# Kernel optimization log

Measured on AMD Instinct MI355X. Metric: run time of the kernel, lower is better.

The kernel has to match this reference:

```python
import jax, jax.numpy as jnp
import numpy as np

COEFS = [1.5, 1.2, 1.0, 0.9, 0.82, 0.69, 0.65, 0.56]  # self.coefs reversed
COMMITMENT_COST = 0.4


def number_to_pair(n):
    if n == 1:
        return (0, 1)
    m = (n - 1) // 2
    e = 1 if (n % 2 == 0) else 0
    return (2 * m + 3 + e - 1, 2 * m + 4 + e - 1)


def build_codebooks(weight, num_levels):
    # Level-l codebook has 2^l vectors, built as sums of pairs of rows of `weight`.
    d = weight.shape[1]
    cbs = []
    prev = None
    for stage in range(1, num_levels + 1):
        i0, i1 = number_to_pair(stage)
        vecs = weight[i0:i1 + 1]            # [2, d]
        if stage == 1:
            cb = vecs
        else:
            cb = (prev[:, None, :] + vecs[None, :, :]).reshape(-1, d)
        cbs.append(cb)
        prev = cb
    return cbs


def quantize(cb, flat):
    dists = (jnp.sum(flat ** 2, axis=1, keepdims=True)
             + jnp.sum(cb ** 2, axis=1)
             - 2.0 * flat @ cb.T)           # [N, K]
    idx = jnp.argmin(dists, axis=1)          # [N]
    return jnp.take(cb, idx, axis=0)         # == one-hot @ cb


def setup_inputs() -> dict:
    key = jax.random.key(0)
    k1, k2 = jax.random.split(key)
    B, d, H, W = 16, 128, 64, 64
    p = 256
    inputs = jax.random.normal(k1, (B, d, H, W), dtype=jnp.float32)
    weight = jax.random.normal(k2, (p, d), dtype=jnp.float32)  # nn.Embedding default N(0,1)
    return {"inputs": inputs, "weight": weight, "num_vectors": 256}


def reference(inputs, weight, num_vectors):
    num_levels = int(np.log2(num_vectors))   # 8
    x = jnp.transpose(inputs, (0, 2, 3, 1))  # [B, H, W, d]
    d = x.shape[-1]
    flat = x.reshape(-1, d)                  # [N, d]
    cbs = build_codebooks(weight, num_levels)

    quant_vecs = []
    losses = []
    for level in range(num_levels):
        q = quantize(cbs[level], flat).reshape(x.shape)
        e_latent = jnp.mean((jax.lax.stop_gradient(q) - x) ** 2)
        q_latent = jnp.mean((jax.lax.stop_gradient(x) - q) ** 2)
        losses.append(COEFS[level] * q_latent + COMMITMENT_COST * e_latent)
        st = x + jax.lax.stop_gradient(q - x)             # straight-through
        quant_vecs.append(jnp.transpose(st, (0, 3, 1, 2)))  # back to [B, d, H, W]

    return jnp.stack(quant_vecs), jnp.stack(losses)
```

## Files before the change

kernel.cpp:

```cpp
#include <hip/hip_runtime.h>

typedef unsigned long long u64;

#define OFF_A      0
#define OFF_DT     512
#define OFF_V0T    1536
#define OFF_BASET  2560
#define OFF_IDX_BYTES 16384
#define OFF_PART_F    135168

__device__ __forceinline__ float warp_sum(float v) {
  #pragma unroll
  for (int off = 32; off > 0; off >>= 1) v += __shfl_down(v, off);
  return v;
}

__global__ __launch_bounds__(64) void build_tables(const float* __restrict__ w,
                                                   float* __restrict__ wsf) {
  const int r0[8] = {0, 3, 4, 5, 6, 7, 8, 9};
  int e = blockIdx.x;
  int t = threadIdx.x;
  if (e < 510) {
    int ep2 = e + 2;
    int L = 31 - __clz(ep2);
    int i = ep2 - (1 << L);
    float acc = 0.f;
    #pragma unroll
    for (int half = 0; half < 2; ++half) {
      int cc = t + half * 64;
      float v = 0.f;
      for (int s = 0; s < L; ++s) {
        int b = (i >> (L - 1 - s)) & 1;
        v += w[(r0[s] + b) * 128 + cc];
      }
      acc += v * v;
    }
    acc = warp_sum(acc);
    if (t == 0) wsf[OFF_A + e] = -0.5f * acc;
  } else {
    #pragma unroll
    for (int half = 0; half < 2; ++half) {
      int cc = t + half * 64;
      float basesum = 0.f;
      #pragma unroll
      for (int s = 0; s < 8; ++s) {
        float w0 = w[r0[s] * 128 + cc];
        float w1 = w[(r0[s] + 1) * 128 + cc];
        wsf[OFF_V0T + cc * 8 + s] = w0;
        wsf[OFF_DT + cc * 8 + s] = w1 - w0;
        basesum += w0;
        wsf[OFF_BASET + s * 128 + cc] = basesum;
      }
    }
  }
}

template <int L, int I, int N>
struct SU {
  static __device__ __forceinline__ void run(const float* __restrict__ Al,
                                             const float* T, const float* S,
                                             float& bs, int& bi) {
    float dot;
    if constexpr (L <= 4) {
      dot = T[I << (4 - L)];
    } else {
      dot = T[I >> (L - 4)] + S[(I & ((1 << (L - 4)) - 1)) << (8 - L)];
    }
    float sc = dot + Al[I];
    if (sc > bs) { bs = sc; bi = I; }
    SU<L, I + 1, N>::run(Al, T, S, bs, bi);
  }
};
template <int L, int N>
struct SU<L, N, N> {
  static __device__ __forceinline__ void run(const float*, const float*, const float*,
                                             float&, int&) {}
};

template <int L>
__device__ __forceinline__ void search_level(const float* __restrict__ A,
                                             const float* T, const float* S,
                                             float& bestsc, int& bestidx) {
  const float* Al = A + ((1 << L) - 2);
  float bs = -3.4e38f;
  int bi = 0;
  SU<L, 0, (1 << L)>::run(Al, T, S, bs, bi);
  bestsc = bs;
  bestidx = bi;
}

__global__ __launch_bounds__(256) void search_kernel(const float* __restrict__ in,
                                                     const float* __restrict__ tbl,
                                                     float* __restrict__ partial,
                                                     u64* __restrict__ idxp) {
  __shared__ float red[4][8];
  int pos = blockIdx.x * 256 + threadIdx.x;
  int b = pos >> 12;
  int hw = pos & 4095;
  const float* xp = in + ((size_t)b << 19) + hw;
  const float4* dT4 = (const float4*)(tbl + OFF_DT);
  const float4* v04 = (const float4*)(tbl + OFF_V0T);

  float qq[8], uu[8];
  #pragma unroll
  for (int k = 0; k < 8; ++k) { qq[k] = 0.f; uu[k] = 0.f; }
  float xx = 0.f;
  #pragma unroll 4
  for (int c = 0; c < 128; ++c) {
    float x = xp[(size_t)c << 12];
    float4 d0 = dT4[2 * c];
    float4 d1 = dT4[2 * c + 1];
    float4 u0 = v04[2 * c];
    float4 u1 = v04[2 * c + 1];
    xx = fmaf(x, x, xx);
    qq[0] = fmaf(x, d0.x, qq[0]); qq[1] = fmaf(x, d0.y, qq[1]);
    qq[2] = fmaf(x, d0.z, qq[2]); qq[3] = fmaf(x, d0.w, qq[3]);
    qq[4] = fmaf(x, d1.x, qq[4]); qq[5] = fmaf(x, d1.y, qq[5]);
    qq[6] = fmaf(x, d1.z, qq[6]); qq[7] = fmaf(x, d1.w, qq[7]);
    uu[0] = fmaf(x, u0.x, uu[0]); uu[1] = fmaf(x, u0.y, uu[1]);
    uu[2] = fmaf(x, u0.z, uu[2]); uu[3] = fmaf(x, u0.w, uu[3]);
    uu[4] = fmaf(x, u1.x, uu[4]); uu[5] = fmaf(x, u1.y, uu[5]);
    uu[6] = fmaf(x, u1.z, uu[6]); uu[7] = fmaf(x, u1.w, uu[7]);
  }

  float T[16], S[16];
  #pragma unroll
  for (int h = 0; h < 16; ++h) {
    float tv = 0.f, sv = 0.f;
    if (h & 8) { tv += qq[0]; sv += qq[4]; }
    if (h & 4) { tv += qq[1]; sv += qq[5]; }
    if (h & 2) { tv += qq[2]; sv += qq[6]; }
    if (h & 1) { tv += qq[3]; sv += qq[7]; }
    T[h] = tv; S[h] = sv;
  }

  const float* A = tbl + OFF_A;
  float bsc[8];
  int bix[8];
  search_level<1>(A, T, S, bsc[0], bix[0]);
  search_level<2>(A, T, S, bsc[1], bix[1]);
  search_level<3>(A, T, S, bsc[2], bix[2]);
  search_level<4>(A, T, S, bsc[3], bix[3]);
  search_level<5>(A, T, S, bsc[4], bix[4]);
  search_level<6>(A, T, S, bsc[5], bix[5]);
  search_level<7>(A, T, S, bsc[6], bix[6]);
  search_level<8>(A, T, S, bsc[7], bix[7]);

  u64 pk = (u64)bix[0] | ((u64)bix[1] << 1) | ((u64)bix[2] << 3) | ((u64)bix[3] << 6) |
           ((u64)bix[4] << 10) | ((u64)bix[5] << 15) | ((u64)bix[6] << 21) |
           ((u64)bix[7] << 28);
  idxp[pos] = pk;

  int wv = threadIdx.x >> 6;
  float P0 = 0.f;
  #pragma unroll
  for (int l = 0; l < 8; ++l) {
    P0 += uu[l];
    float sse = xx - 2.f * (P0 + bsc[l]);
    sse = warp_sum(sse);
    if ((threadIdx.x & 63) == 0) red[wv][l] = sse;
  }
  __syncthreads();
  if (threadIdx.x < 8) {
    int l = threadIdx.x;
    partial[l * 256 + blockIdx.x] = red[0][l] + red[1][l] + red[2][l] + red[3][l];
  }
}

template <int LV>
__device__ __forceinline__ void write_level(const u64* __restrict__ idxp,
                                            const float* __restrict__ tbl,
                                            float* __restrict__ op, int pos) {
  const int SH[9] = {0, 0, 1, 3, 6, 10, 15, 21, 28};
  u64 pk = idxp[pos];
  int idx = (int)((pk >> SH[LV]) & ((1u << LV) - 1));
  float bf[LV];
  #pragma unroll
  for (int s = 0; s < LV; ++s) bf[s] = (float)((idx >> (LV - 1 - s)) & 1);
  const float* bt = tbl + OFF_BASET + (LV - 1) * 128;
  const float4* dT4 = (const float4*)(tbl + OFF_DT);
  #pragma unroll 4
  for (int c = 0; c < 128; ++c) {
    float qv = bt[c];
    float dv[8];
    float4 d0 = dT4[2 * c];
    dv[0] = d0.x; dv[1] = d0.y; dv[2] = d0.z; dv[3] = d0.w;
    if constexpr (LV > 4) {
      float4 d1 = dT4[2 * c + 1];
      dv[4] = d1.x; dv[5] = d1.y; dv[6] = d1.z; dv[7] = d1.w;
    }
    #pragma unroll
    for (int s = 0; s < LV; ++s) qv = fmaf(bf[s], dv[s], qv);
    op[(size_t)c << 12] = qv;
  }
}

__global__ __launch_bounds__(256) void write_kernel(const float* __restrict__ tbl,
                                                    const u64* __restrict__ idxp,
                                                    float* __restrict__ out) {
  int blk = blockIdx.x;
  int hb = blk & 15;
  int bb = (blk >> 4) & 15;
  int L = blk >> 8;
  int hw = hb * 256 + threadIdx.x;
  int pos = (bb << 12) + hw;
  float* op = out + (((size_t)(L * 16 + bb)) << 19) + hw;
  switch (L) {
    case 0: write_level<1>(idxp, tbl, op, pos); break;
    case 1: write_level<2>(idxp, tbl, op, pos); break;
    case 2: write_level<3>(idxp, tbl, op, pos); break;
    case 3: write_level<4>(idxp, tbl, op, pos); break;
    case 4: write_level<5>(idxp, tbl, op, pos); break;
    case 5: write_level<6>(idxp, tbl, op, pos); break;
    case 6: write_level<7>(idxp, tbl, op, pos); break;
    case 7: write_level<8>(idxp, tbl, op, pos); break;
  }
  if (blk == 0 && threadIdx.x < 64) {
    const float CO[8] = {1.5f, 1.2f, 1.0f, 0.9f, 0.82f, 0.69f, 0.65f, 0.56f};
    const float* partial = tbl + OFF_PART_F;
    int t = threadIdx.x;
    int l = t >> 3;
    int j = t & 7;
    float s = 0.f;
    #pragma unroll 4
    for (int k = 0; k < 32; ++k) s += partial[l * 256 + j + k * 8];
    s += __shfl_down(s, 4);
    s += __shfl_down(s, 2);
    s += __shfl_down(s, 1);
    if (j == 0)
      out[67108864ull + l] = (CO[l] + 0.4f) * s * (1.0f / 8388608.0f);
  }
}

extern "C" void kernel_launch(void* const* d_in, const int* in_sizes, int n_in,
                              void* d_out, int out_size, void* d_ws, size_t ws_size,
                              hipStream_t stream) {
  const float* in = (const float*)d_in[0];
  const float* w  = (const float*)d_in[1];
  float* wsf = (float*)d_ws;
  u64* idxp = (u64*)((char*)d_ws + OFF_IDX_BYTES);
  float* partial = wsf + OFF_PART_F;
  float* out = (float*)d_out;

  build_tables<<<511, 64, 0, stream>>>(w, wsf);
  search_kernel<<<256, 256, 0, stream>>>(in, wsf, partial, idxp);
  write_kernel<<<2048, 256, 0, stream>>>(wsf, idxp, out);
}
```

Before: 328.8 us.

## Split channel reduction and level search across waves; vectorize quantized output writes

The search kernel now uses four waves per block, each covering 64 positions. Each wave accumulates a quarter of the channels, the partial sums are reduced through shared memory, and the level searches are divided among the waves. This raises the search grid from 256 to 1024 blocks for more parallelism and memory-level concurrency. The tables are staged in LDS. The write kernel now has each thread produce four adjacent positions with float4 stores, using LDS-cached tables, which cuts the block count to 512. The costs are extra shared-memory traffic, extra barriers, and unbalanced search work across waves.

```diff
diff --git a/kernel.cpp b/kernel.cpp
--- a/kernel.cpp
+++ b/kernel.cpp
@@ -57,9 +57,8 @@
 
 template <int L, int I, int N>
 struct SU {
-  static __device__ __forceinline__ void run(const float* __restrict__ Al,
-                                             const float* T, const float* S,
-                                             float& bs, int& bi) {
+  static __device__ __forceinline__ void run(const float* Al, const float* T,
+                                             const float* S, float& bs, int& bi) {
     float dot;
     if constexpr (L <= 4) {
       dot = T[I << (4 - L)];
@@ -78,10 +77,9 @@
 };
 
 template <int L>
-__device__ __forceinline__ void search_level(const float* __restrict__ A,
-                                             const float* T, const float* S,
-                                             float& bestsc, int& bestidx) {
-  const float* Al = A + ((1 << L) - 2);
+__device__ __forceinline__ void search_level(const float* Al_base, const float* T,
+                                             const float* S, float& bestsc, int& bestidx) {
+  const float* Al = Al_base + ((1 << L) - 2);
   float bs = -3.4e38f;
   int bi = 0;
   SU<L, 0, (1 << L)>::run(Al, T, S, bs, bi);
@@ -93,34 +91,58 @@
                                                      const float* __restrict__ tbl,
                                                      float* __restrict__ partial,
                                                      u64* __restrict__ idxp) {
-  __shared__ float red[4][8];
-  int pos = blockIdx.x * 256 + threadIdx.x;
-  int b = pos >> 12;
-  int hw = pos & 4095;
-  const float* xp = in + ((size_t)b << 19) + hw;
-  const float4* dT4 = (const float4*)(tbl + OFF_DT);
-  const float4* v04 = (const float4*)(tbl + OFF_V0T);
+  __shared__ float dTl[1024];
+  __shared__ float v0l[1024];
+  __shared__ float Al[512];
+  __shared__ float part[256][17];
+  __shared__ float lsc[4][64];
+  __shared__ int   lix[4][64];
+
+  int tid = threadIdx.x;
+  for (int i = tid; i < 1024; i += 256) { dTl[i] = tbl[OFF_DT + i]; v0l[i] = tbl[OFF_V0T + i]; }
+  if (tid < 255) { Al[tid] = tbl[OFF_A + tid]; Al[tid + 255] = tbl[OFF_A + tid + 255]; }
+  __syncthreads();
+
+  int q = tid >> 6;
+  int posl = tid & 63;
+  int gpos = blockIdx.x * 64 + posl;
+  int b = gpos >> 12;
+  int hw = gpos & 4095;
+  const float* xp = in + ((size_t)b << 19) + ((size_t)(q * 32) << 12) + hw;
 
   float qq[8], uu[8];
   #pragma unroll
   for (int k = 0; k < 8; ++k) { qq[k] = 0.f; uu[k] = 0.f; }
   float xx = 0.f;
-  #pragma unroll 4
-  for (int c = 0; c < 128; ++c) {
-    float x = xp[(size_t)c << 12];
-    float4 d0 = dT4[2 * c];
-    float4 d1 = dT4[2 * c + 1];
-    float4 u0 = v04[2 * c];
-    float4 u1 = v04[2 * c + 1];
-    xx = fmaf(x, x, xx);
-    qq[0] = fmaf(x, d0.x, qq[0]); qq[1] = fmaf(x, d0.y, qq[1]);
-    qq[2] = fmaf(x, d0.z, qq[2]); qq[3] = fmaf(x, d0.w, qq[3]);
-    qq[4] = fmaf(x, d1.x, qq[4]); qq[5] = fmaf(x, d1.y, qq[5]);
-    qq[6] = fmaf(x, d1.z, qq[6]); qq[7] = fmaf(x, d1.w, qq[7]);
-    uu[0] = fmaf(x, u0.x, uu[0]); uu[1] = fmaf(x, u0.y, uu[1]);
-    uu[2] = fmaf(x, u0.z, uu[2]); uu[3] = fmaf(x, u0.w, uu[3]);
-    uu[4] = fmaf(x, u1.x, uu[4]); uu[5] = fmaf(x, u1.y, uu[5]);
-    uu[6] = fmaf(x, u1.z, uu[6]); uu[7] = fmaf(x, u1.w, uu[7]);
+  int cbase = q * 32;
+  float xv[16];
+  #pragma unroll
+  for (int g = 0; g < 2; ++g) {
+    #pragma unroll
+    for (int j = 0; j < 16; ++j) xv[j] = xp[(size_t)(g * 16 + j) << 12];
+    #pragma unroll
+    for (int j = 0; j < 16; ++j) {
+      float x = xv[j];
+      int c = cbase + g * 16 + j;
+      xx = fmaf(x, x, xx);
+      #pragma unroll
+      for (int k = 0; k < 8; ++k) {
+        qq[k] = fmaf(x, dTl[c * 8 + k], qq[k]);
+        uu[k] = fmaf(x, v0l[c * 8 + k], uu[k]);
+      }
+    }
+  }
+
+  #pragma unroll
+  for (int k = 0; k < 8; ++k) { part[tid][k] = qq[k]; part[tid][8 + k] = uu[k]; }
+  part[tid][16] = xx;
+  __syncthreads();
+  #pragma unroll
+  for (int p = 1; p < 4; ++p) {
+    int ptn = tid ^ (p << 6);
+    #pragma unroll
+    for (int k = 0; k < 8; ++k) { qq[k] += part[ptn][k]; uu[k] += part[ptn][8 + k]; }
+    xx += part[ptn][16];
   }
 
   float T[16], S[16];
@@ -134,87 +156,92 @@
     T[h] = tv; S[h] = sv;
   }
 
-  const float* A = tbl + OFF_A;
-  float bsc[8];
-  int bix[8];
-  search_level<1>(A, T, S, bsc[0], bix[0]);
-  search_level<2>(A, T, S, bsc[1], bix[1]);
-  search_level<3>(A, T, S, bsc[2], bix[2]);
-  search_level<4>(A, T, S, bsc[3], bix[3]);
-  search_level<5>(A, T, S, bsc[4], bix[4]);
-  search_level<6>(A, T, S, bsc[5], bix[5]);
-  search_level<7>(A, T, S, bsc[6], bix[6]);
-  search_level<8>(A, T, S, bsc[7], bix[7]);
-
-  u64 pk = (u64)bix[0] | ((u64)bix[1] << 1) | ((u64)bix[2] << 3) | ((u64)bix[3] << 6) |
-           ((u64)bix[4] << 10) | ((u64)bix[5] << 15) | ((u64)bix[6] << 21) |
-           ((u64)bix[7] << 28);
-  idxp[pos] = pk;
-
-  int wv = threadIdx.x >> 6;
-  float P0 = 0.f;
-  #pragma unroll
-  for (int l = 0; l < 8; ++l) {
-    P0 += uu[l];
-    float sse = xx - 2.f * (P0 + bsc[l]);
-    sse = warp_sum(sse);
-    if ((threadIdx.x & 63) == 0) red[wv][l] = sse;
-  }
-  __syncthreads();
-  if (threadIdx.x < 8) {
-    int l = threadIdx.x;
-    partial[l * 256 + blockIdx.x] = red[0][l] + red[1][l] + red[2][l] + red[3][l];
+  float bsc[4];
+  int bix[4];
+  if (q == 3) {
+    float bs; int bi;
+    search_level<8>(Al, T, S, bs, bi);
+    lsc[3][posl] = bs; lix[3][posl] = bi;
+  } else if (q == 2) {
+    float bs; int bi;
+    search_level<7>(Al, T, S, bs, bi);
+    lsc[2][posl] = bs; lix[2][posl] = bi;
+  } else if (q == 1) {
+    float bs; int bi;
+    search_level<5>(Al, T, S, bs, bi);
+    lsc[0][posl] = bs; lix[0][posl] = bi;
+    search_level<6>(Al, T, S, bs, bi);
+    lsc[1][posl] = bs; lix[1][posl] = bi;
+  } else {
+    search_level<1>(Al, T, S, bsc[0], bix[0]);
+    search_level<2>(Al, T, S, bsc[1], bix[1]);
+    search_level<3>(Al, T, S, bsc[2], bix[2]);
+    search_level<4>(Al, T, S, bsc[3], bix[3]);
+  }
+  __syncthreads();
+
+  if (q == 0) {
+    float s5 = lsc[0][posl], s6 = lsc[1][posl], s7 = lsc[2][posl], s8 = lsc[3][posl];
+    int i5 = lix[0][posl], i6 = lix[1][posl], i7 = lix[2][posl], i8 = lix[3][posl];
+    u64 pk = (u64)bix[0] | ((u64)bix[1] << 1) | ((u64)bix[2] << 3) | ((u64)bix[3] << 6) |
+             ((u64)i5 << 10) | ((u64)i6 << 15) | ((u64)i7 << 21) | ((u64)i8 << 28);
+    idxp[gpos] = pk;
+    float ball[8] = {bsc[0], bsc[1], bsc[2], bsc[3], s5, s6, s7, s8};
+    float P0 = 0.f;
+    #pragma unroll
+    for (int l = 0; l < 8; ++l) {
+      P0 += uu[l];
+      float sse = xx - 2.f * (P0 + ball[l]);
+      sse = warp_sum(sse);
+      if (tid == 0) partial[l * 1024 + blockIdx.x] = sse;
+    }
   }
 }
 
 template <int LV>
-__device__ __forceinline__ void write_level(const u64* __restrict__ idxp,
-                                            const float* __restrict__ tbl,
-                                            float* __restrict__ op, int pos) {
-  const int SH[9] = {0, 0, 1, 3, 6, 10, 15, 21, 28};
-  u64 pk = idxp[pos];
-  int idx = (int)((pk >> SH[LV]) & ((1u << LV) - 1));
-  float bf[LV];
-  #pragma unroll
-  for (int s = 0; s < LV; ++s) bf[s] = (float)((idx >> (LV - 1 - s)) & 1);
-  const float* bt = tbl + OFF_BASET + (LV - 1) * 128;
-  const float4* dT4 = (const float4*)(tbl + OFF_DT);
-  #pragma unroll 4
+__device__ __forceinline__ void write_level(const float* dTl, const float* btl,
+                                            const u64* __restrict__ idxp, int pos,
+                                            float4* __restrict__ op) {
+  constexpr int SHv = (LV == 1 ? 0 : LV == 2 ? 1 : LV == 3 ? 3 : LV == 4 ? 6 :
+                       LV == 5 ? 10 : LV == 6 ? 15 : LV == 7 ? 21 : 28);
+  float bf[4][LV];
+  #pragma unroll
+  for (int p = 0; p < 4; ++p) {
+    u64 pk = idxp[pos + p];
+    int idx = (int)((pk >> SHv) & ((1u << LV) - 1));
+    #pragma unroll
+    for (int s = 0; s < LV; ++s) bf[p][s] = (float)((idx >> (LV - 1 - s)) & 1);
+  }
+  #pragma unroll 2
   for (int c = 0; c < 128; ++c) {
-    float qv = bt[c];
-    float dv[8];
-    float4 d0 = dT4[2 * c];
-    dv[0] = d0.x; dv[1] = d0.y; dv[2] = d0.z; dv[3] = d0.w;
-    if constexpr (LV > 4) {
-      float4 d1 = dT4[2 * c + 1];
-      dv[4] = d1.x; dv[5] = d1.y; dv[6] = d1.z; dv[7] = d1.w;
-    }
-    #pragma unroll
-    for (int s = 0; s < LV; ++s) qv = fmaf(bf[s], dv[s], qv);
-    op[(size_t)c << 12] = qv;
+    float bt = btl[c];
+    float dv[LV];
+    #pragma unroll
+    for (int s = 0; s < LV; ++s) dv[s] = dTl[c * 8 + s];
+    float q0 = bt, q1 = bt, q2 = bt, q3 = bt;
+    #pragma unroll
+    for (int s = 0; s < LV; ++s) {
+      q0 = fmaf(bf[0][s], dv[s], q0);
+      q1 = fmaf(bf[1][s], dv[s], q1);
+      q2 = fmaf(bf[2][s], dv[s], q2);
+      q3 = fmaf(bf[3][s], dv[s], q3);
+    }
+    float4 r; r.x = q0; r.y = q1; r.z = q2; r.w = q3;
+    op[(size_t)c << 10] = r;
   }
 }
 
 __global__ __launch_bounds__(256) void write_kernel(const float* __restrict__ tbl,
                                                     const u64* __restrict__ idxp,
                                                     float* __restrict__ out) {
+  __shared__ float dTl[1024];
+  __shared__ float btl[128];
   int blk = blockIdx.x;
-  int hb = blk & 15;
-  int bb = (blk >> 4) & 15;
-  int L = blk >> 8;
-  int hw = hb * 256 + threadIdx.x;
-  int pos = (bb << 12) + hw;
-  float* op = out + (((size_t)(L * 16 + bb)) << 19) + hw;
-  switch (L) {
-    case 0: write_level<1>(idxp, tbl, op, pos); break;
-    case 1: write_level<2>(idxp, tbl, op, pos); break;
-    case 2: write_level<3>(idxp, tbl, op, pos); break;
-    case 3: write_level<4>(idxp, tbl, op, pos); break;
-    case 4: write_level<5>(idxp, tbl, op, pos); break;
-    case 5: write_level<6>(idxp, tbl, op, pos); break;
-    case 6: write_level<7>(idxp, tbl, op, pos); break;
-    case 7: write_level<8>(idxp, tbl, op, pos); break;
-  }
+  int L = blk >> 6;
+  for (int i = threadIdx.x; i < 1024; i += 256) dTl[i] = tbl[OFF_DT + i];
+  if (threadIdx.x < 128) btl[threadIdx.x] = tbl[OFF_BASET + L * 128 + threadIdx.x];
+  __syncthreads();
+
   if (blk == 0 && threadIdx.x < 64) {
     const float CO[8] = {1.5f, 1.2f, 1.0f, 0.9f, 0.82f, 0.69f, 0.65f, 0.56f};
     const float* partial = tbl + OFF_PART_F;
@@ -223,12 +250,28 @@
     int j = t & 7;
     float s = 0.f;
     #pragma unroll 4
-    for (int k = 0; k < 32; ++k) s += partial[l * 256 + j + k * 8];
+    for (int k = 0; k < 128; ++k) s += partial[l * 1024 + j + k * 8];
     s += __shfl_down(s, 4);
     s += __shfl_down(s, 2);
     s += __shfl_down(s, 1);
     if (j == 0)
       out[67108864ull + l] = (CO[l] + 0.4f) * s * (1.0f / 8388608.0f);
+  }
+
+  int g = (blk & 63) * 256 + threadIdx.x;
+  int pos = g << 2;
+  int bb = pos >> 12;
+  int hw = pos & 4095;
+  float4* op = (float4*)(out + (((size_t)(L * 16 + bb)) << 19) + hw);
+  switch (L) {
+    case 0: write_level<1>(dTl, btl, idxp, pos, op); break;
+    case 1: write_level<2>(dTl, btl, idxp, pos, op); break;
+    case 2: write_level<3>(dTl, btl, idxp, pos, op); break;
+    case 3: write_level<4>(dTl, btl, idxp, pos, op); break;
+    case 4: write_level<5>(dTl, btl, idxp, pos, op); break;
+    case 5: write_level<6>(dTl, btl, idxp, pos, op); break;
+    case 6: write_level<7>(dTl, btl, idxp, pos, op); break;
+    case 7: write_level<8>(dTl, btl, idxp, pos, op); break;
   }
 }
 
@@ -243,6 +286,6 @@
   float* out = (float*)d_out;
 
   build_tables<<<511, 64, 0, stream>>>(w, wsf);
-  search_kernel<<<256, 256, 0, stream>>>(in, wsf, partial, idxp);
-  write_kernel<<<2048, 256, 0, stream>>>(wsf, idxp, out);
-}
+  search_kernel<<<1024, 256, 0, stream>>>(in, wsf, partial, idxp);
+  write_kernel<<<512, 256, 0, stream>>>(wsf, idxp, out);
+}
```

Result: slower. 352.2 us (+7.1%).

## Fuse search and output-write kernels, stage tables in LDS, last-block loss reduction

Applied to the files above, without the earlier changes.

Merges the search and write kernels into one kernel where each thread computes its eight level indices and directly writes all eight straight-through outputs. This removes the packed-index round trip and a kernel launch. Lookup tables are staged in shared memory, and the final loss reduction runs in the last block to finish, found with an atomic counter. Each thread now does far more work, including 8x the stores, across only 512 blocks of 128 threads, which may reduce parallelism and memory-level concurrency for the write-heavy phase.

```diff
diff --git a/kernel.cpp b/kernel.cpp
--- a/kernel.cpp
+++ b/kernel.cpp
@@ -2,12 +2,12 @@
 
 typedef unsigned long long u64;
 
-#define OFF_A      0
-#define OFF_DT     512
-#define OFF_V0T    1536
-#define OFF_BASET  2560
-#define OFF_IDX_BYTES 16384
-#define OFF_PART_F    135168
+#define OFF_A    0
+#define OFF_DT   512
+#define OFF_V0T  1536
+#define OFF_BTT  2560
+#define OFF_PART 3584
+#define OFF_CNT  7680
 
 __device__ __forceinline__ float warp_sum(float v) {
   #pragma unroll
@@ -49,17 +49,17 @@
         wsf[OFF_V0T + cc * 8 + s] = w0;
         wsf[OFF_DT + cc * 8 + s] = w1 - w0;
         basesum += w0;
-        wsf[OFF_BASET + s * 128 + cc] = basesum;
+        wsf[OFF_BTT + cc * 8 + s] = basesum;
       }
     }
+    if (t == 0) ((int*)wsf)[OFF_CNT] = 0;
   }
 }
 
 template <int L, int I, int N>
 struct SU {
-  static __device__ __forceinline__ void run(const float* __restrict__ Al,
-                                             const float* T, const float* S,
-                                             float& bs, int& bi) {
+  static __device__ __forceinline__ void run(const float* Al, const float* T,
+                                             const float* S, float& bs, int& bi) {
     float dot;
     if constexpr (L <= 4) {
       dot = T[I << (4 - L)];
@@ -78,10 +78,9 @@
 };
 
 template <int L>
-__device__ __forceinline__ void search_level(const float* __restrict__ A,
-                                             const float* T, const float* S,
-                                             float& bestsc, int& bestidx) {
-  const float* Al = A + ((1 << L) - 2);
+__device__ __forceinline__ void search_level(const float* Al_base, const float* T,
+                                             const float* S, float& bestsc, int& bestidx) {
+  const float* Al = Al_base + ((1 << L) - 2);
   float bs = -3.4e38f;
   int bi = 0;
   SU<L, 0, (1 << L)>::run(Al, T, S, bs, bi);
@@ -89,17 +88,33 @@
   bestidx = bi;
 }
 
-__global__ __launch_bounds__(256) void search_kernel(const float* __restrict__ in,
-                                                     const float* __restrict__ tbl,
-                                                     float* __restrict__ partial,
-                                                     u64* __restrict__ idxp) {
-  __shared__ float red[4][8];
-  int pos = blockIdx.x * 256 + threadIdx.x;
-  int b = pos >> 12;
-  int hw = pos & 4095;
+__global__ __launch_bounds__(128) void fused_kernel(const float* __restrict__ in,
+                                                    const float* __restrict__ tbl,
+                                                    float* __restrict__ partial,
+                                                    int* __restrict__ counter,
+                                                    float* __restrict__ out) {
+  __shared__ __align__(16) float dTl[1024];
+  __shared__ __align__(16) float v0l[1024];
+  __shared__ __align__(16) float btl[1024];
+  __shared__ float Al[510];
+  __shared__ float red[2][8];
+  __shared__ int lastflag;
+
+  int tid = threadIdx.x;
+  for (int i = tid; i < 1024; i += 128) {
+    dTl[i] = tbl[OFF_DT + i];
+    v0l[i] = tbl[OFF_V0T + i];
+    btl[i] = tbl[OFF_BTT + i];
+  }
+  for (int i = tid; i < 510; i += 128) Al[i] = tbl[OFF_A + i];
+  __syncthreads();
+
+  int gpos = blockIdx.x * 128 + tid;
+  int b = gpos >> 12;
+  int hw = gpos & 4095;
   const float* xp = in + ((size_t)b << 19) + hw;
-  const float4* dT4 = (const float4*)(tbl + OFF_DT);
-  const float4* v04 = (const float4*)(tbl + OFF_V0T);
+  const float4* dT4 = (const float4*)dTl;
+  const float4* v04 = (const float4*)v0l;
 
   float qq[8], uu[8];
   #pragma unroll
@@ -108,10 +123,8 @@
   #pragma unroll 4
   for (int c = 0; c < 128; ++c) {
     float x = xp[(size_t)c << 12];
-    float4 d0 = dT4[2 * c];
-    float4 d1 = dT4[2 * c + 1];
-    float4 u0 = v04[2 * c];
-    float4 u1 = v04[2 * c + 1];
+    float4 d0 = dT4[2 * c], d1 = dT4[2 * c + 1];
+    float4 u0 = v04[2 * c], u1 = v04[2 * c + 1];
     xx = fmaf(x, x, xx);
     qq[0] = fmaf(x, d0.x, qq[0]); qq[1] = fmaf(x, d0.y, qq[1]);
     qq[2] = fmaf(x, d0.z, qq[2]); qq[3] = fmaf(x, d0.w, qq[3]);
@@ -134,101 +147,78 @@
     T[h] = tv; S[h] = sv;
   }
 
-  const float* A = tbl + OFF_A;
   float bsc[8];
   int bix[8];
-  search_level<1>(A, T, S, bsc[0], bix[0]);
-  search_level<2>(A, T, S, bsc[1], bix[1]);
-  search_level<3>(A, T, S, bsc[2], bix[2]);
-  search_level<4>(A, T, S, bsc[3], bix[3]);
-  search_level<5>(A, T, S, bsc[4], bix[4]);
-  search_level<6>(A, T, S, bsc[5], bix[5]);
-  search_level<7>(A, T, S, bsc[6], bix[6]);
-  search_level<8>(A, T, S, bsc[7], bix[7]);
-
-  u64 pk = (u64)bix[0] | ((u64)bix[1] << 1) | ((u64)bix[2] << 3) | ((u64)bix[3] << 6) |
-           ((u64)bix[4] << 10) | ((u64)bix[5] << 15) | ((u64)bix[6] << 21) |
-           ((u64)bix[7] << 28);
-  idxp[pos] = pk;
-
-  int wv = threadIdx.x >> 6;
+  search_level<1>(Al, T, S, bsc[0], bix[0]);
+  search_level<2>(Al, T, S, bsc[1], bix[1]);
+  search_level<3>(Al, T, S, bsc[2], bix[2]);
+  search_level<4>(Al, T, S, bsc[3], bix[3]);
+  search_level<5>(Al, T, S, bsc[4], bix[4]);
+  search_level<6>(Al, T, S, bsc[5], bix[5]);
+  search_level<7>(Al, T, S, bsc[6], bix[6]);
+  search_level<8>(Al, T, S, bsc[7], bix[7]);
+
+  int wv = tid >> 6;
   float P0 = 0.f;
   #pragma unroll
   for (int l = 0; l < 8; ++l) {
     P0 += uu[l];
     float sse = xx - 2.f * (P0 + bsc[l]);
     sse = warp_sum(sse);
-    if ((threadIdx.x & 63) == 0) red[wv][l] = sse;
-  }
-  __syncthreads();
-  if (threadIdx.x < 8) {
-    int l = threadIdx.x;
-    partial[l * 256 + blockIdx.x] = red[0][l] + red[1][l] + red[2][l] + red[3][l];
-  }
-}
-
-template <int LV>
-__device__ __forceinline__ void write_level(const u64* __restrict__ idxp,
-                                            const float* __restrict__ tbl,
-                                            float* __restrict__ op, int pos) {
-  const int SH[9] = {0, 0, 1, 3, 6, 10, 15, 21, 28};
-  u64 pk = idxp[pos];
-  int idx = (int)((pk >> SH[LV]) & ((1u << LV) - 1));
-  float bf[LV];
-  #pragma unroll
-  for (int s = 0; s < LV; ++s) bf[s] = (float)((idx >> (LV - 1 - s)) & 1);
-  const float* bt = tbl + OFF_BASET + (LV - 1) * 128;
-  const float4* dT4 = (const float4*)(tbl + OFF_DT);
-  #pragma unroll 4
+    if ((tid & 63) == 0) red[wv][l] = sse;
+  }
+  __syncthreads();
+  if (tid < 8) partial[tid * 512 + blockIdx.x] = red[0][tid] + red[1][tid];
+
+  const int TRI[8] = {0, 1, 3, 6, 10, 15, 21, 28};
+  float bf[36];
+  #pragma unroll
+  for (int l = 0; l < 8; ++l) {
+    #pragma unroll
+    for (int s = 0; s < 8; ++s) {
+      if (s <= l) bf[TRI[l] + s] = (float)((bix[l] >> (l - s)) & 1);
+    }
+  }
+
+  const float4* bt4 = (const float4*)btl;
+  size_t obase = ((size_t)b << 19) + hw;
+  #pragma unroll 2
   for (int c = 0; c < 128; ++c) {
-    float qv = bt[c];
-    float dv[8];
-    float4 d0 = dT4[2 * c];
-    dv[0] = d0.x; dv[1] = d0.y; dv[2] = d0.z; dv[3] = d0.w;
-    if constexpr (LV > 4) {
-      float4 d1 = dT4[2 * c + 1];
-      dv[4] = d1.x; dv[5] = d1.y; dv[6] = d1.z; dv[7] = d1.w;
-    }
-    #pragma unroll
-    for (int s = 0; s < LV; ++s) qv = fmaf(bf[s], dv[s], qv);
-    op[(size_t)c << 12] = qv;
-  }
-}
-
-__global__ __launch_bounds__(256) void write_kernel(const float* __restrict__ tbl,
-                                                    const u64* __restrict__ idxp,
-                                                    float* __restrict__ out) {
-  int blk = blockIdx.x;
-  int hb = blk & 15;
-  int bb = (blk >> 4) & 15;
-  int L = blk >> 8;
-  int hw = hb * 256 + threadIdx.x;
-  int pos = (bb << 12) + hw;
-  float* op = out + (((size_t)(L * 16 + bb)) << 19) + hw;
-  switch (L) {
-    case 0: write_level<1>(idxp, tbl, op, pos); break;
-    case 1: write_level<2>(idxp, tbl, op, pos); break;
-    case 2: write_level<3>(idxp, tbl, op, pos); break;
-    case 3: write_level<4>(idxp, tbl, op, pos); break;
-    case 4: write_level<5>(idxp, tbl, op, pos); break;
-    case 5: write_level<6>(idxp, tbl, op, pos); break;
-    case 6: write_level<7>(idxp, tbl, op, pos); break;
-    case 7: write_level<8>(idxp, tbl, op, pos); break;
-  }
-  if (blk == 0 && threadIdx.x < 64) {
-    const float CO[8] = {1.5f, 1.2f, 1.0f, 0.9f, 0.82f, 0.69f, 0.65f, 0.56f};
-    const float* partial = tbl + OFF_PART_F;
-    int t = threadIdx.x;
-    int l = t >> 3;
-    int j = t & 7;
-    float s = 0.f;
-    #pragma unroll 4
-    for (int k = 0; k < 32; ++k) s += partial[l * 256 + j + k * 8];
-    s += __shfl_down(s, 4);
-    s += __shfl_down(s, 2);
-    s += __shfl_down(s, 1);
-    if (j == 0)
-      out[67108864ull + l] = (CO[l] + 0.4f) * s * (1.0f / 8388608.0f);
+    float4 d0 = dT4[2 * c], d1 = dT4[2 * c + 1];
+    float4 t0 = bt4[2 * c], t1 = bt4[2 * c + 1];
+    float dv[8] = {d0.x, d0.y, d0.z, d0.w, d1.x, d1.y, d1.z, d1.w};
+    float bt[8] = {t0.x, t0.y, t0.z, t0.w, t1.x, t1.y, t1.z, t1.w};
+    size_t cbase = obase + ((size_t)c << 12);
+    #pragma unroll
+    for (int l = 0; l < 8; ++l) {
+      float v = bt[l];
+      #pragma unroll
+      for (int s = 0; s < 8; ++s) {
+        if (s <= l) v = fmaf(bf[TRI[l] + s], dv[s], v);
+      }
+      out[cbase + ((size_t)l << 23)] = v;
+    }
+  }
+
+  __threadfence();
+  __syncthreads();
+  if (tid == 0) lastflag = (atomicAdd(counter, 1) == 511);
+  __syncthreads();
+  if (lastflag) {
+    __threadfence();
+    if (tid < 64) {
+      const float CO[8] = {1.5f, 1.2f, 1.0f, 0.9f, 0.82f, 0.69f, 0.65f, 0.56f};
+      int l = tid >> 3;
+      int j = tid & 7;
+      float s = 0.f;
+      #pragma unroll 4
+      for (int k = 0; k < 64; ++k) s += partial[l * 512 + j + k * 8];
+      s += __shfl_down(s, 4);
+      s += __shfl_down(s, 2);
+      s += __shfl_down(s, 1);
+      if (j == 0)
+        out[67108864ull + l] = (CO[l] + 0.4f) * s * (1.0f / 8388608.0f);
+    }
   }
 }
 
@@ -238,11 +228,10 @@
   const float* in = (const float*)d_in[0];
   const float* w  = (const float*)d_in[1];
   float* wsf = (float*)d_ws;
-  u64* idxp = (u64*)((char*)d_ws + OFF_IDX_BYTES);
-  float* partial = wsf + OFF_PART_F;
+  float* partial = wsf + OFF_PART;
+  int* counter = ((int*)wsf) + OFF_CNT;
   float* out = (float*)d_out;
 
   build_tables<<<511, 64, 0, stream>>>(w, wsf);
-  search_kernel<<<256, 256, 0, stream>>>(in, wsf, partial, idxp);
-  write_kernel<<<2048, 256, 0, stream>>>(wsf, idxp, out);
-}
+  fused_kernel<<<512, 128, 0, stream>>>(in, wsf, partial, counter, out);
+}
```

After: 371.8 us. 13.1% more time.
